# Kernel optimization log

Hardware: AMD Instinct MI355X
Metric: run time of the kernel (lower is better)

Reference implementation:

```python
import jax, jax.numpy as jnp
import numpy as np

N_NODES = 50000
N_EDGES = 800000
F_IN = 64
HID = 256
EMB = 128
N_LAYERS = 3


def setup_inputs() -> dict:
    key = jax.random.key(0)
    ks = jax.random.split(key, 20)
    s = lambda i, shape: jax.random.normal(ks[i], shape, dtype=jnp.float32) * 0.05
    inp = {
        'x': jax.random.normal(ks[0], (N_NODES, F_IN), dtype=jnp.float32),
        'edge_index': jax.random.randint(ks[1], (2, N_EDGES), 0, N_NODES, dtype=jnp.int64),
        # node_encoder: Linear(F_IN,HID) -> ReLU -> Dropout -> Linear(HID,HID)
        'W1': s(2, (F_IN, HID)), 'b1': s(3, (HID,)),
        'W2': s(4, (HID, HID)), 'b2': s(5, (HID,)),
        # stacked GCN layer weights [L,HID,HID], biases [L,HID]
        'conv_W': s(6, (N_LAYERS, HID, HID)), 'conv_b': s(7, (N_LAYERS, HID)),
        # graph_projection: Linear(2H,H) -> ReLU -> Dropout -> Linear(H,EMB)
        'Wg1': s(8, (2 * HID, HID)), 'bg1': s(9, (HID,)),
        'Wg2': s(10, (HID, EMB)), 'bg2': s(11, (EMB,)),
        # decoder node_projection: Linear(EMB,H) -> ReLU -> Linear(H,H)
        'Wd1': s(12, (EMB, HID)), 'bd1': s(13, (HID,)),
        'Wd2': s(14, (HID, HID)), 'bd2': s(15, (HID,)),
    }
    return inp


def _forward(x, edge_index, W1, b1, W2, b2, conv_W, conv_b, Wg1, bg1, Wg2, bg2, Wd1, bd1, Wd2, bd2):
    N = x.shape[0]
    # node encoder (dropout is identity in eval)
    h = jax.nn.relu(x @ W1 + b1) @ W2 + b2  # [N,H]

    # GCN normalization with self-loops (PyG GCNConv defaults)
    self_idx = jnp.arange(N, dtype=edge_index.dtype)
    src = jnp.concatenate([edge_index[0], self_idx])  # [E+N]
    dst = jnp.concatenate([edge_index[1], self_idx])
    deg = jax.ops.segment_sum(jnp.ones_like(dst, dtype=h.dtype), dst, num_segments=N)
    dinv = jnp.where(deg > 0, jax.lax.rsqrt(deg), 0.0)
    norm = (dinv[src] * dinv[dst])[:, None]  # [E+N,1]

    for l in range(N_LAYERS):
        hw = h @ conv_W[l]                              # [N,H]
        msg = hw[src] * norm                            # gather + scale
        h = jax.ops.segment_sum(msg, dst, num_segments=N) + conv_b[l]
        h = jax.nn.relu(h)

    # global mean + max pool (single graph)
    graph_rep = jnp.concatenate([h.mean(axis=0), h.max(axis=0)])[None, :]  # [1,2H]
    graph_embedding = jax.nn.relu(graph_rep @ Wg1 + bg1) @ Wg2 + bg2       # [1,EMB]

    # decoder: project graph embedding, broadcast to all nodes, score edges
    v = jax.nn.relu(graph_embedding @ Wd1 + bd1) @ Wd2 + bd2  # [1,H]
    node_emb = jnp.broadcast_to(v, (N, v.shape[1]))           # [N,H]
    row, col = edge_index[0], edge_index[1]
    edge_logits = jnp.sum(node_emb[row] * node_emb[col], axis=1)  # [E]
    edge_probs = jax.nn.sigmoid(edge_logits)
    return graph_embedding, edge_probs


def reference(x, edge_index, W1, b1, W2, b2, conv_W, conv_b, Wg1, bg1, Wg2, bg2, Wd1, bd1, Wd2, bd2):
    return _forward(x, edge_index, W1, b1, W2, b2, conv_W, conv_b, Wg1, bg1, Wg2, bg2, Wd1, bd1, Wd2, bd2)
```

## Files before the change

kernel.cpp:

```cpp
#include <hip/hip_runtime.h>
#include <hip/hip_bf16.h>


typedef __attribute__((ext_vector_type(8))) short bf16x8;
typedef __attribute__((ext_vector_type(4))) float f32x4;
typedef __attribute__((ext_vector_type(2))) float f32x2;

#define FP8_SCALE 32.0f
#define FP8_INV (1.0f / 32.0f)

__device__ __forceinline__ ushort f2bf(float f) {
  union { float f; unsigned u; } v; v.f = f;
  unsigned r = v.u + 0x7FFF + ((v.u >> 16) & 1);
  return (ushort)(r >> 16);
}
__device__ __forceinline__ float bf2f(ushort b) {
  union { unsigned u; float f; } v; v.u = ((unsigned)b) << 16;
  return v.f;
}


__global__ void init_detect_kernel(const int* __restrict__ ei, int* __restrict__ flag,
                                   int* __restrict__ cnt8, int N8) {
  int i = blockIdx.x * 256 + threadIdx.x;
  if (i < N8) cnt8[i] = 0;
  if (blockIdx.x == 0 && threadIdx.x == 0) {
    int all0 = 1;
    for (int k = 0; k < 128; ++k) {
      if (ei[2 * k + 1] != 0) { all0 = 0; break; }
    }
    flag[0] = all0;
  }
}

__global__ void count_kernel(const int* __restrict__ ei, const int* __restrict__ flag,
                             int* __restrict__ cnt8, int* __restrict__ rank, int E, int N) {
  int e = blockIdx.x * 256 + threadIdx.x;
  if (e >= E) return;
  int d;
  if (flag[0]) d = (int)((const long long*)ei)[(size_t)E + e];
  else         d = ei[(size_t)E + e];
  rank[e] = atomicAdd(&cnt8[(size_t)(blockIdx.x & 7) * N + d], 1);
}


__global__ __launch_bounds__(256) void bsum_kernel(const int* __restrict__ cnt8,
                                                   int* __restrict__ cnt,
                                                   int* __restrict__ bsum, int N) {
  __shared__ int red[4];
  int t = threadIdx.x;
  int i = blockIdx.x * 256 + t;
  int v = 0;
  if (i < N) {
#pragma unroll
    for (int c = 0; c < 8; ++c) v += cnt8[(size_t)c * N + i];
    cnt[i] = v;
  }
  for (int off = 32; off > 0; off >>= 1) v += __shfl_down(v, off, 64);
  if ((t & 63) == 0) red[t >> 6] = v;
  __syncthreads();
  if (t == 0) bsum[blockIdx.x] = red[0] + red[1] + red[2] + red[3];
}

__global__ __launch_bounds__(256) void bscan_kernel(const int* __restrict__ bsum,
                                                    int* __restrict__ boff,
                                                    int* __restrict__ rowptr, int B, int N) {
  __shared__ int s[256];
  int t = threadIdx.x;
  int v = (t < B) ? bsum[t] : 0;
  s[t] = v;
  __syncthreads();
  for (int off = 1; off < 256; off <<= 1) {
    int x = s[t];
    int add = (t >= off) ? s[t - off] : 0;
    __syncthreads();
    s[t] = x + add;
    __syncthreads();
  }
  if (t < B) boff[t] = s[t] - v;
  if (t == 255) rowptr[N] = s[255];
}

__global__ __launch_bounds__(256) void rowptr_kernel(const int* __restrict__ cnt,
                                                     const int* __restrict__ cnt8,
                                                     const int* __restrict__ boff,
                                                     int* __restrict__ rowptr,
                                                     int* __restrict__ base8,
                                                     float* __restrict__ dinv, int N) {
  __shared__ int s[256];
  int t = threadIdx.x;
  int i = blockIdx.x * 256 + t;
  int v = (i < N) ? cnt[i] : 0;
  s[t] = v;
  __syncthreads();
  for (int off = 1; off < 256; off <<= 1) {
    int x = s[t];
    int add = (t >= off) ? s[t - off] : 0;
    __syncthreads();
    s[t] = x + add;
    __syncthreads();
  }
  if (i < N) {
    int rp = boff[blockIdx.x] + s[t] - v;
    rowptr[i] = rp;
    int run = rp;
#pragma unroll
    for (int c = 0; c < 8; ++c) {
      base8[(size_t)c * N + i] = run;
      run += cnt8[(size_t)c * N + i];
    }
    dinv[i] = rsqrtf((float)(v + 1));
  }
}

__global__ void scatter_kernel(const int* __restrict__ ei, const int* __restrict__ flag,
                               const int* __restrict__ rank, const int* __restrict__ base8,
                               ushort* __restrict__ col, int E, int N) {
  int e = blockIdx.x * 256 + threadIdx.x;
  if (e >= E) return;
  int s, d;
  if (flag[0]) {
    const long long* e64 = (const long long*)ei;
    s = (int)e64[e];
    d = (int)e64[(size_t)E + e];
  } else {
    s = ei[e];
    d = ei[(size_t)E + e];
  }
  int c = (e >> 8) & 7;
  int pos = base8[(size_t)c * N + d] + rank[e];
  col[pos] = (ushort)s;
}


__global__ void prep_kernel(const float* __restrict__ x, ushort* __restrict__ xb,
                            int n, int npad,
                            const float* __restrict__ W1, ushort* __restrict__ Wp1,
                            const float* __restrict__ W2, ushort* __restrict__ Wp2,
                            const float* __restrict__ cW, ushort* __restrict__ Wpc) {
  int b = blockIdx.x;
  int nCvt = (npad + 255) / 256;
  if (b < nCvt) {
    int i = b * 256 + threadIdx.x;
    if (i < n) xb[i] = f2bf(x[i]);
    else if (i < npad) xb[i] = 0;
    return;
  }
  b -= nCvt;
  const float* W;
  ushort* Wp;
  int K;
  if (b < 8) { W = W1; Wp = Wp1; K = 64; }
  else if (b < 40) { W = W2; Wp = Wp2; K = 256; b -= 8; }
  else {
    int l = (b - 40) >> 5;
    W = cW + (size_t)l * 256 * 256;
    Wp = Wpc + (size_t)l * 8 * 16 * 64 * 8;
    K = 256;
    b -= 40 + l * 32;
  }
  int idx = b * 256 + threadIdx.x;
  int total = (K >> 5) * 16 * 64;
  if (idx >= total) return;
  int lane = idx & 63;
  int cb = (idx >> 6) & 15;
  int ks = idx >> 10;
  int nn = cb * 16 + (lane & 15);
  int kbase = ks * 32 + (lane >> 4) * 8;
#pragma unroll
  for (int i = 0; i < 8; ++i)
    Wp[(size_t)idx * 8 + i] = f2bf(W[(size_t)(kbase + i) * 256 + nn]);
}


template <int NKS>
__global__ __launch_bounds__(256) void gemm_mfma_kernel(
    const ushort* __restrict__ A,
    const ushort* __restrict__ Wp,
    const float* __restrict__ bias,
    const float* __restrict__ scale,
    ushort* __restrict__ C,
    unsigned char* __restrict__ C8,
    int M, int relu) {
  constexpr int K = NKS * 32;
  int t = threadIdx.x;
  int lane = t & 63, wave = t >> 6;
  int l15 = lane & 15, lk = lane >> 4;
  int row0 = blockIdx.x * 64;

  f32x4 acc[4][4];
#pragma unroll
  for (int rb = 0; rb < 4; ++rb)
#pragma unroll
    for (int cb = 0; cb < 4; ++cb) acc[rb][cb] = (f32x4){0.f, 0.f, 0.f, 0.f};

  const ushort* abase[4];
#pragma unroll
  for (int rb = 0; rb < 4; ++rb)
    abase[rb] = A + (size_t)(row0 + rb * 16 + l15) * K + lk * 8;
  const ushort* bbase = Wp + ((size_t)(wave * 4) * 64 + lane) * 8;

#pragma unroll
  for (int ks = 0; ks < NKS; ++ks) {
    bf16x8 a[4], b[4];
#pragma unroll
    for (int rb = 0; rb < 4; ++rb)
      a[rb] = *reinterpret_cast<const bf16x8*>(abase[rb] + ks * 32);
#pragma unroll
    for (int cb = 0; cb < 4; ++cb)
      b[cb] = *reinterpret_cast<const bf16x8*>(bbase + ((size_t)ks * 16 + cb) * 64 * 8);
#pragma unroll
    for (int rb = 0; rb < 4; ++rb)
#pragma unroll
      for (int cb = 0; cb < 4; ++cb)
        acc[rb][cb] = __builtin_amdgcn_mfma_f32_16x16x32_bf16(a[rb], b[cb], acc[rb][cb], 0, 0, 0);
  }

  float bv[4];
#pragma unroll
  for (int cb = 0; cb < 4; ++cb)
    bv[cb] = bias ? bias[wave * 64 + cb * 16 + l15] : 0.f;

#pragma unroll
  for (int rb = 0; rb < 4; ++rb) {
    int rbase = row0 + rb * 16 + lk * 4;
#pragma unroll
    for (int r = 0; r < 4; ++r) {
      int row = rbase + r;
      if (row >= M) continue;
      float sc = scale ? scale[row] : 1.f;
#pragma unroll
      for (int cb = 0; cb < 4; ++cb) {
        float v = acc[rb][cb][r] + bv[cb];
        if (relu) v = fmaxf(v, 0.f);
        v *= sc;
        int colIdx = wave * 64 + cb * 16 + l15;
        if (C8) {
          float vq = fminf(fmaxf(v * FP8_SCALE, -448.f), 448.f);
          unsigned p = __builtin_amdgcn_cvt_pk_fp8_f32(vq, vq, 0, false);
          C8[(size_t)row * 256 + colIdx] = (unsigned char)(p & 0xff);
        } else {
          C[(size_t)row * 256 + colIdx] = f2bf(v);
        }
      }
    }
  }
}


__global__ __launch_bounds__(64) void mp_kernel(const unsigned char* __restrict__ hw8,
                                                const int* __restrict__ rowptr,
                                                const ushort* __restrict__ col,
                                                const float* __restrict__ dinv,
                                                const float* __restrict__ bias,
                                                ushort* __restrict__ hout) {
  int n = blockIdx.x;
  int t = threadIdx.x;
  const unsigned* hw32 = reinterpret_cast<const unsigned*>(hw8);
  unsigned ws = hw32[(size_t)n * 64 + t];
  f32x2 lo = __builtin_amdgcn_cvt_pk_f32_fp8(ws, false);
  f32x2 hi = __builtin_amdgcn_cvt_pk_f32_fp8(ws, true);
  float ax = lo[0], ay = lo[1], az = hi[0], aw = hi[1];
  int beg = rowptr[n], end = rowptr[n + 1];
  int j = beg;
  for (; j + 16 <= end; j += 16) {
    int ss[16];
    unsigned ww[16];
#pragma unroll
    for (int q = 0; q < 16; ++q) ss[q] = col[j + q];
#pragma unroll
    for (int q = 0; q < 16; ++q) ww[q] = hw32[(size_t)ss[q] * 64 + t];
#pragma unroll
    for (int q = 0; q < 16; ++q) {
      f32x2 lq = __builtin_amdgcn_cvt_pk_f32_fp8(ww[q], false);
      f32x2 hq = __builtin_amdgcn_cvt_pk_f32_fp8(ww[q], true);
      ax += lq[0]; ay += lq[1]; az += hq[0]; aw += hq[1];
    }
  }
  for (; j + 4 <= end; j += 4) {
    int s0 = col[j], s1 = col[j + 1], s2 = col[j + 2], s3 = col[j + 3];
    unsigned w0 = hw32[(size_t)s0 * 64 + t];
    unsigned w1 = hw32[(size_t)s1 * 64 + t];
    unsigned w2 = hw32[(size_t)s2 * 64 + t];
    unsigned w3 = hw32[(size_t)s3 * 64 + t];
    f32x2 l0 = __builtin_amdgcn_cvt_pk_f32_fp8(w0, false);
    f32x2 h0 = __builtin_amdgcn_cvt_pk_f32_fp8(w0, true);
    f32x2 l1 = __builtin_amdgcn_cvt_pk_f32_fp8(w1, false);
    f32x2 h1 = __builtin_amdgcn_cvt_pk_f32_fp8(w1, true);
    f32x2 l2 = __builtin_amdgcn_cvt_pk_f32_fp8(w2, false);
    f32x2 h2 = __builtin_amdgcn_cvt_pk_f32_fp8(w2, true);
    f32x2 l3 = __builtin_amdgcn_cvt_pk_f32_fp8(w3, false);
    f32x2 h3 = __builtin_amdgcn_cvt_pk_f32_fp8(w3, true);
    ax += (l0[0] + l1[0]) + (l2[0] + l3[0]);
    ay += (l0[1] + l1[1]) + (l2[1] + l3[1]);
    az += (h0[0] + h1[0]) + (h2[0] + h3[0]);
    aw += (h0[1] + h1[1]) + (h2[1] + h3[1]);
  }
  for (; j < end; ++j) {
    int s = col[j];
    unsigned wv = hw32[(size_t)s * 64 + t];
    f32x2 l2 = __builtin_amdgcn_cvt_pk_f32_fp8(wv, false);
    f32x2 h2 = __builtin_amdgcn_cvt_pk_f32_fp8(wv, true);
    ax += l2[0]; ay += l2[1]; az += h2[0]; aw += h2[1];
  }
  float dn = dinv[n] * FP8_INV;
  float4 bv = *reinterpret_cast<const float4*>(bias + t * 4);
  ushort4 o;
  o.x = f2bf(fmaxf(fmaf(dn, ax, bv.x), 0.f));
  o.y = f2bf(fmaxf(fmaf(dn, ay, bv.y), 0.f));
  o.z = f2bf(fmaxf(fmaf(dn, az, bv.z), 0.f));
  o.w = f2bf(fmaxf(fmaf(dn, aw, bv.w), 0.f));
  *reinterpret_cast<ushort4*>(hout + (size_t)n * 256 + t * 4) = o;
}


__global__ __launch_bounds__(256) void pool_partial_kernel(const ushort* __restrict__ h,
                                                           float* __restrict__ psum,
                                                           float* __restrict__ pmax, int N) {
  __shared__ float ssum[4][256];
  __shared__ float smax[4][256];
  int t = threadIdx.x;
  int w = t >> 6, l = t & 63;
  int gw = blockIdx.x * 4 + w;
  float s0 = 0.f, s1 = 0.f, s2 = 0.f, s3 = 0.f;
  float m0 = 0.f, m1 = 0.f, m2 = 0.f, m3 = 0.f;
  const ushort4 z = {0, 0, 0, 0};
  for (int r = gw; r < N; r += 8192) {
    ushort4 v[8];
#pragma unroll
    for (int j = 0; j < 8; ++j) {
      int rj = r + j * 1024;
      v[j] = (rj < N) ? *reinterpret_cast<const ushort4*>(h + (size_t)rj * 256 + l * 4) : z;
    }
#pragma unroll
    for (int j = 0; j < 8; ++j) {
      float a0 = bf2f(v[j].x), a1 = bf2f(v[j].y), a2 = bf2f(v[j].z), a3 = bf2f(v[j].w);
      s0 += a0; s1 += a1; s2 += a2; s3 += a3;
      m0 = fmaxf(m0, a0); m1 = fmaxf(m1, a1); m2 = fmaxf(m2, a2); m3 = fmaxf(m3, a3);
    }
  }
  ssum[w][l * 4] = s0; ssum[w][l * 4 + 1] = s1; ssum[w][l * 4 + 2] = s2; ssum[w][l * 4 + 3] = s3;
  smax[w][l * 4] = m0; smax[w][l * 4 + 1] = m1; smax[w][l * 4 + 2] = m2; smax[w][l * 4 + 3] = m3;
  __syncthreads();
  float s = ssum[0][t] + ssum[1][t] + ssum[2][t] + ssum[3][t];
  float m = fmaxf(fmaxf(smax[0][t], smax[1][t]), fmaxf(smax[2][t], smax[3][t]));
  psum[(size_t)blockIdx.x * 256 + t] = s;
  pmax[(size_t)blockIdx.x * 256 + t] = m;
}

__global__ __launch_bounds__(256) void pool_reduce_kernel(const float* __restrict__ psum,
                                                          const float* __restrict__ pmax,
                                                          float* __restrict__ pooled2) {
  int t = threadIdx.x;
  int g = blockIdx.x;
  if (g < 8) {
    const float* base = psum + (size_t)(g * 32) * 256 + t;
    float acc = 0.f;
#pragma unroll
    for (int i = 0; i < 32; i += 4)
      acc += (base[(size_t)i * 256] + base[(size_t)(i + 1) * 256]) +
             (base[(size_t)(i + 2) * 256] + base[(size_t)(i + 3) * 256]);
    pooled2[g * 256 + t] = acc;
  } else {
    const float* base = pmax + (size_t)((g - 8) * 32) * 256 + t;
    float mx = 0.f;
#pragma unroll
    for (int i = 0; i < 32; i += 4)
      mx = fmaxf(mx, fmaxf(fmaxf(base[(size_t)i * 256], base[(size_t)(i + 1) * 256]),
                           fmaxf(base[(size_t)(i + 2) * 256], base[(size_t)(i + 3) * 256])));
    pooled2[g * 256 + t] = mx;
  }
}


__global__ __launch_bounds__(1024) void head_kernel(const float* __restrict__ pooled2,
                                                    const float* __restrict__ Wg1, const float* __restrict__ bg1,
                                                    const float* __restrict__ Wg2, const float* __restrict__ bg2,
                                                    const float* __restrict__ Wd1, const float* __restrict__ bd1,
                                                    const float* __restrict__ Wd2, const float* __restrict__ bd2,
                                                    float* __restrict__ out_ge, float* __restrict__ s_out, int N) {
  __shared__ float gr[512];
  __shared__ float part[4][256];
  __shared__ float t1[256];
  __shared__ float ge[128];
  __shared__ float t2[256];
  __shared__ float vv[256];
  __shared__ float red[4];
  int t = threadIdx.x;
  float* pf = &part[0][0];

  if (t < 256) {
    float sm = 0.f;
#pragma unroll
    for (int g = 0; g < 8; ++g) sm += pooled2[g * 256 + t];
    gr[t] = sm / (float)N;
  } else if (t < 512) {
    int c = t - 256;
    float mx = 0.f;
#pragma unroll
    for (int g = 8; g < 16; ++g) mx = fmaxf(mx, pooled2[g * 256 + c]);
    gr[256 + c] = mx;
  }
  __syncthreads();

  {
    int kg = t >> 8, c = t & 255, k0 = kg * 128;
    float a0 = 0, a1 = 0, a2 = 0, a3 = 0, a4 = 0, a5 = 0, a6 = 0, a7 = 0;
    for (int k = k0; k < k0 + 128; k += 8) {
      a0 = fmaf(gr[k + 0], Wg1[(size_t)(k + 0) * 256 + c], a0);
      a1 = fmaf(gr[k + 1], Wg1[(size_t)(k + 1) * 256 + c], a1);
      a2 = fmaf(gr[k + 2], Wg1[(size_t)(k + 2) * 256 + c], a2);
      a3 = fmaf(gr[k + 3], Wg1[(size_t)(k + 3) * 256 + c], a3);
      a4 = fmaf(gr[k + 4], Wg1[(size_t)(k + 4) * 256 + c], a4);
      a5 = fmaf(gr[k + 5], Wg1[(size_t)(k + 5) * 256 + c], a5);
      a6 = fmaf(gr[k + 6], Wg1[(size_t)(k + 6) * 256 + c], a6);
      a7 = fmaf(gr[k + 7], Wg1[(size_t)(k + 7) * 256 + c], a7);
    }
    part[kg][c] = ((a0 + a1) + (a2 + a3)) + ((a4 + a5) + (a6 + a7));
  }
  __syncthreads();
  if (t < 256) t1[t] = fmaxf(part[0][t] + part[1][t] + part[2][t] + part[3][t] + bg1[t], 0.f);
  __syncthreads();

  {
    int kg = t >> 7, c = t & 127, k0 = kg * 32;
    float a0 = 0, a1 = 0, a2 = 0, a3 = 0;
    for (int k = k0; k < k0 + 32; k += 4) {
      a0 = fmaf(t1[k + 0], Wg2[(size_t)(k + 0) * 128 + c], a0);
      a1 = fmaf(t1[k + 1], Wg2[(size_t)(k + 1) * 128 + c], a1);
      a2 = fmaf(t1[k + 2], Wg2[(size_t)(k + 2) * 128 + c], a2);
      a3 = fmaf(t1[k + 3], Wg2[(size_t)(k + 3) * 128 + c], a3);
    }
    pf[kg * 128 + c] = (a0 + a1) + (a2 + a3);
  }
  __syncthreads();
  if (t < 128) {
    float s = bg2[t];
#pragma unroll
    for (int g = 0; g < 8; ++g) s += pf[g * 128 + t];
    ge[t] = s;
    out_ge[t] = s;
  }
  __syncthreads();

  {
    int kg = t >> 8, c = t & 255, k0 = kg * 32;
    float a0 = 0, a1 = 0, a2 = 0, a3 = 0;
    for (int k = k0; k < k0 + 32; k += 4) {
      a0 = fmaf(ge[k + 0], Wd1[(size_t)(k + 0) * 256 + c], a0);
      a1 = fmaf(ge[k + 1], Wd1[(size_t)(k + 1) * 256 + c], a1);
      a2 = fmaf(ge[k + 2], Wd1[(size_t)(k + 2) * 256 + c], a2);
      a3 = fmaf(ge[k + 3], Wd1[(size_t)(k + 3) * 256 + c], a3);
    }
    part[kg][c] = (a0 + a1) + (a2 + a3);
  }
  __syncthreads();
  if (t < 256) t2[t] = fmaxf(part[0][t] + part[1][t] + part[2][t] + part[3][t] + bd1[t], 0.f);
  __syncthreads();

  {
    int kg = t >> 8, c = t & 255, k0 = kg * 64;
    float a0 = 0, a1 = 0, a2 = 0, a3 = 0, a4 = 0, a5 = 0, a6 = 0, a7 = 0;
    for (int k = k0; k < k0 + 64; k += 8) {
      a0 = fmaf(t2[k + 0], Wd2[(size_t)(k + 0) * 256 + c], a0);
      a1 = fmaf(t2[k + 1], Wd2[(size_t)(k + 1) * 256 + c], a1);
      a2 = fmaf(t2[k + 2], Wd2[(size_t)(k + 2) * 256 + c], a2);
      a3 = fmaf(t2[k + 3], Wd2[(size_t)(k + 3) * 256 + c], a3);
      a4 = fmaf(t2[k + 4], Wd2[(size_t)(k + 4) * 256 + c], a4);
      a5 = fmaf(t2[k + 5], Wd2[(size_t)(k + 5) * 256 + c], a5);
      a6 = fmaf(t2[k + 6], Wd2[(size_t)(k + 6) * 256 + c], a6);
      a7 = fmaf(t2[k + 7], Wd2[(size_t)(k + 7) * 256 + c], a7);
    }
    part[kg][c] = ((a0 + a1) + (a2 + a3)) + ((a4 + a5) + (a6 + a7));
  }
  __syncthreads();
  if (t < 256) vv[t] = part[0][t] + part[1][t] + part[2][t] + part[3][t] + bd2[t];
  __syncthreads();

  if (t < 256) {
    float p = vv[t] * vv[t];
    for (int off = 32; off > 0; off >>= 1) p += __shfl_down(p, off, 64);
    if ((t & 63) == 0) red[t >> 6] = p;
  }
  __syncthreads();
  if (t == 0) {
    float ssq = red[0] + red[1] + red[2] + red[3];
    s_out[0] = 1.f / (1.f + expf(-ssq));
  }
}

__global__ void fill_kernel(float* __restrict__ out, const float* __restrict__ s_out, int E) {
  int i = (blockIdx.x * 256 + threadIdx.x) * 4;
  if (i + 4 <= E) {
    float s = s_out[0];
    *reinterpret_cast<float4*>(out + i) = make_float4(s, s, s, s);
  } else {
    for (int j = i; j < E; ++j) out[j] = s_out[0];
  }
}


extern "C" void kernel_launch(void* const* d_in, const int* in_sizes, int n_in,
                              void* d_out, int out_size, void* d_ws, size_t ws_size,
                              hipStream_t stream) {
  const float* x   = (const float*)d_in[0];
  const int*   ei  = (const int*)d_in[1];
  const float* W1  = (const float*)d_in[2];
  const float* b1  = (const float*)d_in[3];
  const float* W2  = (const float*)d_in[4];
  const float* b2  = (const float*)d_in[5];
  const float* cW  = (const float*)d_in[6];
  const float* cb  = (const float*)d_in[7];
  const float* Wg1 = (const float*)d_in[8];
  const float* bg1 = (const float*)d_in[9];
  const float* Wg2 = (const float*)d_in[10];
  const float* bg2 = (const float*)d_in[11];
  const float* Wd1 = (const float*)d_in[12];
  const float* bd1 = (const float*)d_in[13];
  const float* Wd2 = (const float*)d_in[14];
  const float* bd2 = (const float*)d_in[15];
  float* out = (float*)d_out;

  int N = in_sizes[0] / 64;
  int E = in_sizes[1] / 2;
  int Mpad = (N + 63) & ~63;
  int B = (N + 255) / 256;

  size_t off = 0;
  auto walloc = [&](size_t bytes) -> void* {
    void* p = (char*)d_ws + off;
    off += (bytes + 511) & ~(size_t)511;
    return p;
  };
  ushort* hA    = (ushort*)walloc((size_t)Mpad * 256 * 2);
  ushort* hB    = (ushort*)walloc((size_t)Mpad * 256 * 2);
  unsigned char* hA8 = (unsigned char*)walloc((size_t)Mpad * 256);
  ushort* xb    = (ushort*)walloc((size_t)Mpad * 64 * 2);
  ushort* Wp1   = (ushort*)walloc((size_t)2 * 16 * 64 * 8 * 2);
  ushort* Wp2   = (ushort*)walloc((size_t)8 * 16 * 64 * 8 * 2);
  ushort* Wpc   = (ushort*)walloc((size_t)3 * 8 * 16 * 64 * 8 * 2);
  int*   cnt8   = (int*)walloc((size_t)8 * N * 4);
  int*   cnt    = (int*)walloc((size_t)N * 4);
  int*   rowptr = (int*)walloc(((size_t)N + 1) * 4);
  int*   base8  = (int*)walloc((size_t)8 * N * 4);
  int*   rank   = (int*)walloc((size_t)E * 4);
  float* dinv   = (float*)walloc((size_t)N * 4);
  ushort* col   = (ushort*)walloc((size_t)E * 2);
  int*   bsum   = (int*)walloc(256 * 4);
  int*   boff   = (int*)walloc(256 * 4);
  float* psum   = (float*)walloc((size_t)256 * 256 * 4);
  float* pmax   = (float*)walloc((size_t)256 * 256 * 4);
  float* pooled2= (float*)walloc(16 * 256 * 4);
  float* s_out  = (float*)walloc(512);
  int*   flag   = (int*)walloc(512);

  init_detect_kernel<<<(8 * N + 255) / 256, 256, 0, stream>>>(ei, flag, cnt8, 8 * N);
  count_kernel<<<(E + 255) / 256, 256, 0, stream>>>(ei, flag, cnt8, rank, E, N);
  bsum_kernel<<<B, 256, 0, stream>>>(cnt8, cnt, bsum, N);
  bscan_kernel<<<1, 256, 0, stream>>>(bsum, boff, rowptr, B, N);
  rowptr_kernel<<<B, 256, 0, stream>>>(cnt, cnt8, boff, rowptr, base8, dinv, N);
  scatter_kernel<<<(E + 255) / 256, 256, 0, stream>>>(ei, flag, rank, base8, col, E, N);

  int nCvt = (Mpad * 64 + 255) / 256;
  prep_kernel<<<nCvt + 8 + 32 + 96, 256, 0, stream>>>(x, xb, N * 64, Mpad * 64,
                                                      W1, Wp1, W2, Wp2, cW, Wpc);

  int gblocks = Mpad / 64;
  gemm_mfma_kernel<2><<<gblocks, 256, 0, stream>>>(xb, Wp1, b1, nullptr, hA, nullptr, N, 1);
  gemm_mfma_kernel<8><<<gblocks, 256, 0, stream>>>(hA, Wp2, b2, nullptr, hB, nullptr, N, 0);
  for (int l = 0; l < 3; ++l) {
    gemm_mfma_kernel<8><<<gblocks, 256, 0, stream>>>(
        hB, Wpc + (size_t)l * 8 * 16 * 64 * 8, nullptr, dinv, nullptr, hA8, N, 0);
    mp_kernel<<<N, 64, 0, stream>>>(hA8, rowptr, col, dinv, cb + (size_t)l * 256, hB);
  }
  pool_partial_kernel<<<256, 256, 0, stream>>>(hB, psum, pmax, N);
  pool_reduce_kernel<<<16, 256, 0, stream>>>(psum, pmax, pooled2);
  head_kernel<<<1, 1024, 0, stream>>>(pooled2, Wg1, bg1, Wg2, bg2, Wd1, bd1, Wd2, bd2, out, s_out, N);
  fill_kernel<<<(E + 1023) / 1024, 256, 0, stream>>>(out + 128, s_out, E);
}
```

Before: 346.1 us.

## Fuse x conversion into first GEMM, merge scatter with weight packing, fold pool reduce

```diff
diff --git a/kernel.cpp b/kernel.cpp
--- a/kernel.cpp
+++ b/kernel.cpp
@@ -34,88 +34,8 @@
 }
 
 __global__ void count_kernel(const int* __restrict__ ei, const int* __restrict__ flag,
-                             int* __restrict__ cnt8, int* __restrict__ rank, int E, int N) {
-  int e = blockIdx.x * 256 + threadIdx.x;
-  if (e >= E) return;
-  int d;
-  if (flag[0]) d = (int)((const long long*)ei)[(size_t)E + e];
-  else         d = ei[(size_t)E + e];
-  rank[e] = atomicAdd(&cnt8[(size_t)(blockIdx.x & 7) * N + d], 1);
-}
-
-
-__global__ __launch_bounds__(256) void bsum_kernel(const int* __restrict__ cnt8,
-                                                   int* __restrict__ cnt,
-                                                   int* __restrict__ bsum, int N) {
-  __shared__ int red[4];
-  int t = threadIdx.x;
-  int i = blockIdx.x * 256 + t;
-  int v = 0;
-  if (i < N) {
-#pragma unroll
-    for (int c = 0; c < 8; ++c) v += cnt8[(size_t)c * N + i];
-    cnt[i] = v;
-  }
-  for (int off = 32; off > 0; off >>= 1) v += __shfl_down(v, off, 64);
-  if ((t & 63) == 0) red[t >> 6] = v;
-  __syncthreads();
-  if (t == 0) bsum[blockIdx.x] = red[0] + red[1] + red[2] + red[3];
-}
-
-__global__ __launch_bounds__(256) void bscan_kernel(const int* __restrict__ bsum,
-                                                    int* __restrict__ boff,
-                                                    int* __restrict__ rowptr, int B, int N) {
-  __shared__ int s[256];
-  int t = threadIdx.x;
-  int v = (t < B) ? bsum[t] : 0;
-  s[t] = v;
-  __syncthreads();
-  for (int off = 1; off < 256; off <<= 1) {
-    int x = s[t];
-    int add = (t >= off) ? s[t - off] : 0;
-    __syncthreads();
-    s[t] = x + add;
-    __syncthreads();
-  }
-  if (t < B) boff[t] = s[t] - v;
-  if (t == 255) rowptr[N] = s[255];
-}
-
-__global__ __launch_bounds__(256) void rowptr_kernel(const int* __restrict__ cnt,
-                                                     const int* __restrict__ cnt8,
-                                                     const int* __restrict__ boff,
-                                                     int* __restrict__ rowptr,
-                                                     int* __restrict__ base8,
-                                                     float* __restrict__ dinv, int N) {
-  __shared__ int s[256];
-  int t = threadIdx.x;
-  int i = blockIdx.x * 256 + t;
-  int v = (i < N) ? cnt[i] : 0;
-  s[t] = v;
-  __syncthreads();
-  for (int off = 1; off < 256; off <<= 1) {
-    int x = s[t];
-    int add = (t >= off) ? s[t - off] : 0;
-    __syncthreads();
-    s[t] = x + add;
-    __syncthreads();
-  }
-  if (i < N) {
-    int rp = boff[blockIdx.x] + s[t] - v;
-    rowptr[i] = rp;
-    int run = rp;
-#pragma unroll
-    for (int c = 0; c < 8; ++c) {
-      base8[(size_t)c * N + i] = run;
-      run += cnt8[(size_t)c * N + i];
-    }
-    dinv[i] = rsqrtf((float)(v + 1));
-  }
-}
-
-__global__ void scatter_kernel(const int* __restrict__ ei, const int* __restrict__ flag,
-                               const int* __restrict__ rank, const int* __restrict__ base8,
-                               ushort* __restrict__ col, int E, int N) {
+                             int* __restrict__ cnt8, int* __restrict__ rank,
+                             unsigned* __restrict__ pairs, int E, int N) {
   int e = blockIdx.x * 256 + threadIdx.x;
   if (e >= E) return;
   int s, d;
@@ -127,26 +47,101 @@
     s = ei[e];
     d = ei[(size_t)E + e];
   }
-  int c = (e >> 8) & 7;
-  int pos = base8[(size_t)c * N + d] + rank[e];
-  col[pos] = (ushort)s;
-}
-
-
-__global__ void prep_kernel(const float* __restrict__ x, ushort* __restrict__ xb,
-                            int n, int npad,
-                            const float* __restrict__ W1, ushort* __restrict__ Wp1,
-                            const float* __restrict__ W2, ushort* __restrict__ Wp2,
-                            const float* __restrict__ cW, ushort* __restrict__ Wpc) {
+  rank[e] = atomicAdd(&cnt8[(size_t)(blockIdx.x & 7) * N + d], 1);
+  pairs[e] = (unsigned)s | ((unsigned)d << 16);
+}
+
+
+__global__ __launch_bounds__(256) void bsum_kernel(const int* __restrict__ cnt8,
+                                                   int* __restrict__ cnt,
+                                                   int* __restrict__ bsum, int N) {
+  __shared__ int red[4];
+  int t = threadIdx.x;
+  int i = blockIdx.x * 256 + t;
+  int v = 0;
+  if (i < N) {
+#pragma unroll
+    for (int c = 0; c < 8; ++c) v += cnt8[(size_t)c * N + i];
+    cnt[i] = v;
+  }
+  for (int off = 32; off > 0; off >>= 1) v += __shfl_down(v, off, 64);
+  if ((t & 63) == 0) red[t >> 6] = v;
+  __syncthreads();
+  if (t == 0) bsum[blockIdx.x] = red[0] + red[1] + red[2] + red[3];
+}
+
+__global__ __launch_bounds__(256) void bscan_kernel(const int* __restrict__ bsum,
+                                                    int* __restrict__ boff,
+                                                    int* __restrict__ rowptr, int B, int N) {
+  __shared__ int s[256];
+  int t = threadIdx.x;
+  int v = (t < B) ? bsum[t] : 0;
+  s[t] = v;
+  __syncthreads();
+  for (int off = 1; off < 256; off <<= 1) {
+    int x = s[t];
+    int add = (t >= off) ? s[t - off] : 0;
+    __syncthreads();
+    s[t] = x + add;
+    __syncthreads();
+  }
+  if (t < B) boff[t] = s[t] - v;
+  if (t == 255) rowptr[N] = s[255];
+}
+
+__global__ __launch_bounds__(256) void rowptr_kernel(const int* __restrict__ cnt,
+                                                     const int* __restrict__ cnt8,
+                                                     const int* __restrict__ boff,
+                                                     int* __restrict__ rowptr,
+                                                     int* __restrict__ base8,
+                                                     float* __restrict__ dinv, int N) {
+  __shared__ int s[256];
+  int t = threadIdx.x;
+  int i = blockIdx.x * 256 + t;
+  int v = (i < N) ? cnt[i] : 0;
+  s[t] = v;
+  __syncthreads();
+  for (int off = 1; off < 256; off <<= 1) {
+    int x = s[t];
+    int add = (t >= off) ? s[t - off] : 0;
+    __syncthreads();
+    s[t] = x + add;
+    __syncthreads();
+  }
+  if (i < N) {
+    int rp = boff[blockIdx.x] + s[t] - v;
+    rowptr[i] = rp;
+    int run = rp;
+#pragma unroll
+    for (int c = 0; c < 8; ++c) {
+      base8[(size_t)c * N + i] = run;
+      run += cnt8[(size_t)c * N + i];
+    }
+    dinv[i] = rsqrtf((float)(v + 1));
+  }
+}
+
+
+__global__ void scatter_pack_kernel(const unsigned* __restrict__ pairs,
+                                    const int* __restrict__ rank,
+                                    const int* __restrict__ base8,
+                                    ushort* __restrict__ col, int E, int N, int nScat,
+                                    const float* __restrict__ W1, ushort* __restrict__ Wp1,
+                                    const float* __restrict__ W2, ushort* __restrict__ Wp2,
+                                    const float* __restrict__ cW, ushort* __restrict__ Wpc) {
   int b = blockIdx.x;
-  int nCvt = (npad + 255) / 256;
-  if (b < nCvt) {
-    int i = b * 256 + threadIdx.x;
-    if (i < n) xb[i] = f2bf(x[i]);
-    else if (i < npad) xb[i] = 0;
+  if (b < nScat) {
+    int e = b * 256 + threadIdx.x;
+    if (e >= E) return;
+    unsigned p = pairs[e];
+    int s = p & 0xffff;
+    int d = p >> 16;
+    int c = (e >> 8) & 7;
+    int pos = base8[(size_t)c * N + d] + rank[e];
+    col[pos] = (ushort)s;
     return;
   }
-  b -= nCvt;
+  b -= nScat;
   const float* W;
   ushort* Wp;
   int K;
@@ -173,9 +168,9 @@
 }
 
 
-template <int NKS>
+template <int NKS, bool AF32>
 __global__ __launch_bounds__(256) void gemm_mfma_kernel(
-    const ushort* __restrict__ A,
+    const void* __restrict__ Av,
     const ushort* __restrict__ Wp,
     const float* __restrict__ bias,
     const float* __restrict__ scale,
@@ -195,17 +190,34 @@
     for (int cb = 0; cb < 4; ++cb) acc[rb][cb] = (f32x4){0.f, 0.f, 0.f, 0.f};
 
   const ushort* abase[4];
-#pragma unroll
-  for (int rb = 0; rb < 4; ++rb)
-    abase[rb] = A + (size_t)(row0 + rb * 16 + l15) * K + lk * 8;
+  const float* afbase[4];
+#pragma unroll
+  for (int rb = 0; rb < 4; ++rb) {
+    int arow = row0 + rb * 16 + l15;
+    if (AF32) arow = min(arow, M - 1);
+    if (AF32) afbase[rb] = (const float*)Av + (size_t)arow * K + lk * 8;
+    else      abase[rb] = (const ushort*)Av + (size_t)arow * K + lk * 8;
+  }
   const ushort* bbase = Wp + ((size_t)(wave * 4) * 64 + lane) * 8;
 
 #pragma unroll
   for (int ks = 0; ks < NKS; ++ks) {
     bf16x8 a[4], b[4];
 #pragma unroll
-    for (int rb = 0; rb < 4; ++rb)
-      a[rb] = *reinterpret_cast<const bf16x8*>(abase[rb] + ks * 32);
+    for (int rb = 0; rb < 4; ++rb) {
+      if (AF32) {
+        float4 f0 = *reinterpret_cast<const float4*>(afbase[rb] + ks * 32);
+        float4 f1 = *reinterpret_cast<const float4*>(afbase[rb] + ks * 32 + 4);
+        bf16x8 av;
+        av[0] = (short)f2bf(f0.x); av[1] = (short)f2bf(f0.y);
+        av[2] = (short)f2bf(f0.z); av[3] = (short)f2bf(f0.w);
+        av[4] = (short)f2bf(f1.x); av[5] = (short)f2bf(f1.y);
+        av[6] = (short)f2bf(f1.z); av[7] = (short)f2bf(f1.w);
+        a[rb] = av;
+      } else {
+        a[rb] = *reinterpret_cast<const bf16x8*>(abase[rb] + ks * 32);
+      }
+    }
 #pragma unroll
     for (int cb = 0; cb < 4; ++cb)
       b[cb] = *reinterpret_cast<const bf16x8*>(bbase + ((size_t)ks * 16 + cb) * 64 * 8);
@@ -348,32 +360,9 @@
   pmax[(size_t)blockIdx.x * 256 + t] = m;
 }
 
-__global__ __launch_bounds__(256) void pool_reduce_kernel(const float* __restrict__ psum,
-                                                          const float* __restrict__ pmax,
-                                                          float* __restrict__ pooled2) {
-  int t = threadIdx.x;
-  int g = blockIdx.x;
-  if (g < 8) {
-    const float* base = psum + (size_t)(g * 32) * 256 + t;
-    float acc = 0.f;
-#pragma unroll
-    for (int i = 0; i < 32; i += 4)
-      acc += (base[(size_t)i * 256] + base[(size_t)(i + 1) * 256]) +
-             (base[(size_t)(i + 2) * 256] + base[(size_t)(i + 3) * 256]);
-    pooled2[g * 256 + t] = acc;
-  } else {
-    const float* base = pmax + (size_t)((g - 8) * 32) * 256 + t;
-    float mx = 0.f;
-#pragma unroll
-    for (int i = 0; i < 32; i += 4)
-      mx = fmaxf(mx, fmaxf(fmaxf(base[(size_t)i * 256], base[(size_t)(i + 1) * 256]),
-                           fmaxf(base[(size_t)(i + 2) * 256], base[(size_t)(i + 3) * 256])));
-    pooled2[g * 256 + t] = mx;
-  }
-}
-
-
-__global__ __launch_bounds__(1024) void head_kernel(const float* __restrict__ pooled2,
+
+__global__ __launch_bounds__(1024) void head_kernel(const float* __restrict__ psum,
+                                                    const float* __restrict__ pmax,
                                                     const float* __restrict__ Wg1, const float* __restrict__ bg1,
                                                     const float* __restrict__ Wg2, const float* __restrict__ bg2,
                                                     const float* __restrict__ Wd1, const float* __restrict__ bd1,
@@ -389,18 +378,32 @@
   int t = threadIdx.x;
   float* pf = &part[0][0];
 
-  if (t < 256) {
-    float sm = 0.f;
-#pragma unroll
-    for (int g = 0; g < 8; ++g) sm += pooled2[g * 256 + t];
-    gr[t] = sm / (float)N;
-  } else if (t < 512) {
-    int c = t - 256;
-    float mx = 0.f;
-#pragma unroll
-    for (int g = 8; g < 16; ++g) mx = fmaxf(mx, pooled2[g * 256 + c]);
-    gr[256 + c] = mx;
-  }
+  {
+    int kg = t >> 8, c = t & 255;
+    const float* base = psum + (size_t)(kg * 64) * 256 + c;
+    float a = 0.f;
+#pragma unroll
+    for (int i = 0; i < 64; i += 4)
+      a += (base[(size_t)i * 256] + base[(size_t)(i + 1) * 256]) +
+           (base[(size_t)(i + 2) * 256] + base[(size_t)(i + 3) * 256]);
+    part[kg][c] = a;
+  }
+  __syncthreads();
+  if (t < 256) gr[t] = (part[0][t] + part[1][t] + part[2][t] + part[3][t]) / (float)N;
+  __syncthreads();
+  {
+    int kg = t >> 8, c = t & 255;
+    const float* base = pmax + (size_t)(kg * 64) * 256 + c;
+    float m = 0.f;
+#pragma unroll
+    for (int i = 0; i < 64; i += 4)
+      m = fmaxf(m, fmaxf(fmaxf(base[(size_t)i * 256], base[(size_t)(i + 1) * 256]),
+                         fmaxf(base[(size_t)(i + 2) * 256], base[(size_t)(i + 3) * 256])));
+    part[kg][c] = m;
+  }
+  __syncthreads();
+  if (t < 256)
+    gr[256 + t] = fmaxf(fmaxf(part[0][t], part[1][t]), fmaxf(part[2][t], part[3][t]));
   __syncthreads();
 
   {
@@ -535,7 +538,6 @@
   ushort* hA    = (ushort*)walloc((size_t)Mpad * 256 * 2);
   ushort* hB    = (ushort*)walloc((size_t)Mpad * 256 * 2);
   unsigned char* hA8 = (unsigned char*)walloc((size_t)Mpad * 256);
-  ushort* xb    = (ushort*)walloc((size_t)Mpad * 64 * 2);
   ushort* Wp1   = (ushort*)walloc((size_t)2 * 16 * 64 * 8 * 2);
   ushort* Wp2   = (ushort*)walloc((size_t)8 * 16 * 64 * 8 * 2);
   ushort* Wpc   = (ushort*)walloc((size_t)3 * 8 * 16 * 64 * 8 * 2);
@@ -544,37 +546,35 @@
   int*   rowptr = (int*)walloc(((size_t)N + 1) * 4);
   int*   base8  = (int*)walloc((size_t)8 * N * 4);
   int*   rank   = (int*)walloc((size_t)E * 4);
+  unsigned* pairs = (unsigned*)walloc((size_t)E * 4);
   float* dinv   = (float*)walloc((size_t)N * 4);
   ushort* col   = (ushort*)walloc((size_t)E * 2);
   int*   bsum   = (int*)walloc(256 * 4);
   int*   boff   = (int*)walloc(256 * 4);
   float* psum   = (float*)walloc((size_t)256 * 256 * 4);
   float* pmax   = (float*)walloc((size_t)256 * 256 * 4);
-  float* pooled2= (float*)walloc(16 * 256 * 4);
   float* s_out  = (float*)walloc(512);
   int*   flag   = (int*)walloc(512);
 
   init_detect_kernel<<<(8 * N + 255) / 256, 256, 0, stream>>>(ei, flag, cnt8, 8 * N);
-  count_kernel<<<(E + 255) / 256, 256, 0, stream>>>(ei, flag, cnt8, rank, E, N);
+  count_kernel<<<(E + 255) / 256, 256, 0, stream>>>(ei, flag, cnt8, rank, pairs, E, N);
   bsum_kernel<<<B, 256, 0, stream>>>(cnt8, cnt, bsum, N);
   bscan_kernel<<<1, 256, 0, stream>>>(bsum, boff, rowptr, B, N);
   rowptr_kernel<<<B, 256, 0, stream>>>(cnt, cnt8, boff, rowptr, base8, dinv, N);
-  scatter_kernel<<<(E + 255) / 256, 256, 0, stream>>>(ei, flag, rank, base8, col, E, N);
-
-  int nCvt = (Mpad * 64 + 255) / 256;
-  prep_kernel<<<nCvt + 8 + 32 + 96, 256, 0, stream>>>(x, xb, N * 64, Mpad * 64,
-                                                      W1, Wp1, W2, Wp2, cW, Wpc);
+  int nScat = (E + 255) / 256;
+  scatter_pack_kernel<<<nScat + 8 + 32 + 96, 256, 0, stream>>>(
+      pairs, rank, base8, col, E, N, nScat, W1, Wp1, W2, Wp2, cW, Wpc);
 
   int gblocks = Mpad / 64;
-  gemm_mfma_kernel<2><<<gblocks, 256, 0, stream>>>(xb, Wp1, b1, nullptr, hA, nullptr, N, 1);
-  gemm_mfma_kernel<8><<<gblocks, 256, 0, stream>>>(hA, Wp2, b2, nullptr, hB, nullptr, N, 0);
+  gemm_mfma_kernel<2, true><<<gblocks, 256, 0, stream>>>(x, Wp1, b1, nullptr, hA, nullptr, N, 1);
+  gemm_mfma_kernel<8, false><<<gblocks, 256, 0, stream>>>(hA, Wp2, b2, nullptr, hB, nullptr, N, 0);
   for (int l = 0; l < 3; ++l) {
-    gemm_mfma_kernel<8><<<gblocks, 256, 0, stream>>>(
+    gemm_mfma_kernel<8, false><<<gblocks, 256, 0, stream>>>(
         hB, Wpc + (size_t)l * 8 * 16 * 64 * 8, nullptr, dinv, nullptr, hA8, N, 0);
     mp_kernel<<<N, 64, 0, stream>>>(hA8, rowptr, col, dinv, cb + (size_t)l * 256, hB);
   }
   pool_partial_kernel<<<256, 256, 0, stream>>>(hB, psum, pmax, N);
-  pool_reduce_kernel<<<16, 256, 0, stream>>>(psum, pmax, pooled2);
-  head_kernel<<<1, 1024, 0, stream>>>(pooled2, Wg1, bg1, Wg2, bg2, Wd1, bd1, Wd2, bd2, out, s_out, N);
+  head_kernel<<<1, 1024, 0, stream>>>(psum, pmax, Wg1, bg1, Wg2, bg2, Wd1, bd1, Wd2, bd2,
+                                      out, s_out, N);
   fill_kernel<<<(E + 1023) / 1024, 256, 0, stream>>>(out + 128, s_out, E);
 }
```

New measurement: 346.5 us. Within noise of the previous version (+0.1%).
